# Kernel optimization log

Measured on AMD Instinct MI355X. Metric: run time of the kernel, lower is better.

Reference implementation:

```python
import jax, jax.numpy as jnp
import numpy as np

EPS = 1e-5

def layernorm(x, g, b):
    mu = jnp.mean(x, axis=-1, keepdims=True)
    var = jnp.mean((x - mu) ** 2, axis=-1, keepdims=True)
    return (x - mu) * jax.lax.rsqrt(var + EPS) * g + b

def cswin_attn(q, k, v, lepe_w, lepe_b, H, W, H_sp, W_sp, num_heads):
    # q,k,v: (B, L, C) with C = branch dim
    B, L, C = q.shape
    d = C // num_heads
    nH, nW = H // H_sp, W // W_sp
    def to_win(t):
        t = t.transpose(0, 2, 1).reshape(B, C, nH, H_sp, nW, W_sp)
        t = t.transpose(0, 2, 4, 3, 5, 1).reshape(B * nH * nW, H_sp * W_sp, num_heads, d)
        return t.transpose(0, 2, 1, 3)  # (Bw, h, N, d)
    kw = to_win(k)
    vw = to_win(v)
    # q windows as images for LePE depthwise conv
    qi = q.transpose(0, 2, 1).reshape(B, C, nH, H_sp, nW, W_sp)
    qi = qi.transpose(0, 2, 4, 1, 3, 5).reshape(B * nH * nW, C, H_sp, W_sp)
    lepe = jax.lax.conv_general_dilated(qi, lepe_w, (1, 1), 'SAME',
                                        feature_group_count=C,
                                        dimension_numbers=('NCHW', 'OIHW', 'NCHW'))
    lepe = lepe + lepe_b[None, :, None, None]
    lepe = lepe.reshape(-1, num_heads, d, H_sp * W_sp).transpose(0, 1, 3, 2)
    qw = qi.reshape(-1, num_heads, d, H_sp * W_sp).transpose(0, 1, 3, 2) * (float(d) ** -0.5)
    attn = jax.nn.softmax(jnp.einsum('whnd,whmd->whnm', qw, kw), axis=-1)
    out = jnp.einsum('whnm,whmd->whnd', attn, vw) + lepe  # (Bw, h, N, d)
    out = out.transpose(0, 2, 1, 3).reshape(B, nH, nW, H_sp, W_sp, C)
    out = out.transpose(0, 1, 3, 2, 4, 5).reshape(B, H * W, C)
    return out

def setup_inputs() -> dict:
    key = jax.random.key(0)
    ks = jax.random.split(key, 20)
    B, C, H, W = 8, 128, 64, 64
    ch_z = 512
    hid = 4 * C
    Cb = C // 2  # branch dim
    s = lambda fin: (1.0 / np.sqrt(fin))
    inp = {
        'x': jax.random.normal(ks[0], (B, C, H, W), jnp.float32),
        'z': jax.random.normal(ks[1], (B, ch_z), jnp.float32),
        'ln1_g': jnp.ones((C,), jnp.float32), 'ln1_b': jnp.zeros((C,), jnp.float32),
        'ln2_g': jnp.ones((C,), jnp.float32), 'ln2_b': jnp.zeros((C,), jnp.float32),
        'Wz1': jax.random.normal(ks[2], (C, ch_z), jnp.float32) * s(ch_z),
        'Wz2': jax.random.normal(ks[3], (C, ch_z), jnp.float32) * s(ch_z),
        'Wqkv': jax.random.normal(ks[4], (3 * C, C), jnp.float32) * s(C),
        'Wproj': jax.random.normal(ks[5], (C, C), jnp.float32) * s(C),
        'bproj': jnp.zeros((C,), jnp.float32),
        'lepe_w0': jax.random.normal(ks[6], (Cb, 1, 3, 3), jnp.float32) * (1.0 / 3.0),
        'lepe_b0': jnp.zeros((Cb,), jnp.float32),
        'lepe_w1': jax.random.normal(ks[7], (Cb, 1, 3, 3), jnp.float32) * (1.0 / 3.0),
        'lepe_b1': jnp.zeros((Cb,), jnp.float32),
        'W1': jax.random.normal(ks[8], (hid, C), jnp.float32) * s(C),
        'b1': jnp.zeros((hid,), jnp.float32),
        'W2': jax.random.normal(ks[9], (C, hid), jnp.float32) * s(hid),
        'b2': jnp.zeros((C,), jnp.float32),
    }
    return inp

def reference(x, z, ln1_g, ln1_b, ln2_g, ln2_b, Wz1, Wz2, Wqkv, Wproj, bproj,
              lepe_w0, lepe_b0, lepe_w1, lepe_b1, W1, b1, W2, b2):
    B, C, H, W = x.shape
    nh = 4  # num_heads // 2 per branch
    ss = 8  # split_size
    Cb = C // 2
    xf = x.reshape(B, C, H * W).transpose(0, 2, 1)  # (B, L, C)
    # code-conditioned attention branch
    z1 = z @ Wz1.T  # (B, C)
    h1 = layernorm(xf, ln1_g, ln1_b) + z1[:, None, :]
    qkv = (h1 @ Wqkv.T).reshape(B, H * W, 3, C).transpose(2, 0, 1, 3)  # (3, B, L, C)
    q, k, v = qkv[0], qkv[1], qkv[2]
    x1 = cswin_attn(q[..., :Cb], k[..., :Cb], v[..., :Cb], lepe_w0, lepe_b0, H, W, H, ss, nh)
    x2 = cswin_attn(q[..., Cb:], k[..., Cb:], v[..., Cb:], lepe_w1, lepe_b1, H, W, ss, W, nh)
    att = jnp.concatenate([x1, x2], axis=2) @ Wproj.T + bproj
    xf = xf + att
    # code-conditioned MLP branch
    z2 = z @ Wz2.T
    h2 = layernorm(xf, ln2_g, ln2_b) + z2[:, None, :]
    mlp = jax.nn.gelu(h2 @ W1.T + b1, approximate=False) @ W2.T + b2
    xf = xf + mlp
    return xf.transpose(0, 2, 1).reshape(B, C, H, W)
```

## Files before the change

### kernel.cpp

```cpp
#include <hip/hip_runtime.h>
#include <cstddef>

__device__ __forceinline__ float b2f(unsigned short u) {
  return __uint_as_float(((unsigned int)u) << 16);
}
__device__ __forceinline__ unsigned short f2b(float f) {
  unsigned int u = __float_as_uint(f);
  u = u + 0x7FFFu + ((u >> 16) & 1u);
  return (unsigned short)(u >> 16);
}
__device__ __forceinline__ unsigned int cvtpk(float lo, float hi) {
  unsigned int r;
  asm("v_cvt_pk_bf16_f32 %0, %1, %2" : "=v"(r) : "v"(lo), "v"(hi));
  return r;
}
__device__ __forceinline__ float gelu_exact(float x) {
  return 0.5f * x * (1.0f + erff(x * 0.70710678118654752f));
}

#if defined(__has_builtin)
#if __has_builtin(__builtin_amdgcn_exp2f)
#define EXP2(x) __builtin_amdgcn_exp2f(x)
#else
#define EXP2(x) __expf((x) * 0.6931471805599453f)
#endif
#else
#define EXP2(x) __expf((x) * 0.6931471805599453f)
#endif

typedef __attribute__((ext_vector_type(8))) short bf16x8;
typedef __attribute__((ext_vector_type(4))) float f32x4;

__device__ __forceinline__ unsigned int dtype_flag(const unsigned short* gref) {
  return (gref[0] == 0x3F80u) ? 1u : 0u;
}

struct Ptrs18 { const void* p[18]; };
__constant__ const int c_off[19] = {
    0, 4096, 4224, 4352, 4480, 4608, 70144, 135680, 184832, 201216,
    201344, 201920, 201984, 202560, 202624, 268160, 268672, 334208, 334336};

__global__ __launch_bounds__(256) void k_convert(Ptrs18 ptrs,
                                                 unsigned short* __restrict__ dst) {
  int idx = blockIdx.x * 256 + threadIdx.x;
  if (idx >= 334336) return;
  unsigned int flag = dtype_flag((const unsigned short*)ptrs.p[1]);
  int i = 0;
#pragma unroll
  for (int t = 1; t < 18; ++t) i += (idx >= c_off[t]);
  int local = idx - c_off[i];
  if (flag) dst[idx] = ((const unsigned short*)ptrs.p[i])[local];
  else      dst[idx] = f2b(((const float*)ptrs.p[i])[local]);
}

__global__ __launch_bounds__(256) void k_transpose_in(const void* __restrict__ x,
                                                      const unsigned short* __restrict__ gref,
                                                      float* __restrict__ xf) {
  __shared__ float t[32][33];
  unsigned int flag = dtype_flag(gref);
  int b = blockIdx.z;
  int l0 = blockIdx.x * 32, c0 = blockIdx.y * 32;
  int tx = threadIdx.x & 31, ty = threadIdx.x >> 5;
#pragma unroll
  for (int i = 0; i < 32; i += 8) {
    size_t gi = ((size_t)b * 128 + c0 + ty + i) * 4096 + l0 + tx;
    t[ty + i][tx] = flag ? b2f(((const unsigned short*)x)[gi]) : ((const float*)x)[gi];
  }
  __syncthreads();
#pragma unroll
  for (int i = 0; i < 32; i += 8)
    xf[((size_t)b * 4096 + l0 + ty + i) * 128 + c0 + tx] = t[tx][ty + i];
}

__global__ __launch_bounds__(256) void k_zmm(const unsigned short* __restrict__ z,
                                             const unsigned short* __restrict__ Wz1,
                                             const unsigned short* __restrict__ Wz2,
                                             float* __restrict__ zz) {
  __shared__ float sz[512];
  int b = blockIdx.x, tid = threadIdx.x;
  sz[tid]       = b2f(z[b * 512 + tid]);
  sz[tid + 256] = b2f(z[b * 512 + 256 + tid]);
  __syncthreads();
  const unsigned short* W = (tid < 128) ? Wz1 : Wz2;
  int c = tid & 127;
  const unsigned short* wr = W + c * 512;
  float acc = 0.f;
  for (int k = 0; k < 512; k += 4) {
    ushort4 wv = *(const ushort4*)&wr[k];
    acc += b2f(wv.x) * sz[k] + b2f(wv.y) * sz[k + 1] + b2f(wv.z) * sz[k + 2] + b2f(wv.w) * sz[k + 3];
  }
  zz[b * 256 + tid] = acc;
}

__global__ __launch_bounds__(256) void k_ln(const float* __restrict__ x,
                                            const unsigned short* __restrict__ g,
                                            const unsigned short* __restrict__ bb,
                                            const float* __restrict__ zz, int zsel,
                                            unsigned short* __restrict__ out) {
  int row = blockIdx.x * 4 + (threadIdx.x >> 6);
  int lane = threadIdx.x & 63;
  int b = row >> 12;
  const float* xr = x + (size_t)row * 128;
  float2 v = *(const float2*)&xr[lane * 2];
  float s = v.x + v.y, s2 = v.x * v.x + v.y * v.y;
#pragma unroll
  for (int m = 32; m; m >>= 1) {
    s += __shfl_xor(s, m, 64);
    s2 += __shfl_xor(s2, m, 64);
  }
  float mu = s * 0.0078125f;
  float var = s2 * 0.0078125f - mu * mu;
  float rstd = rsqrtf(var + 1e-5f);
  int c = lane * 2;
  const float* zr = zz + b * 256 + zsel * 128;
  float ox = (v.x - mu) * rstd * b2f(g[c])     + b2f(bb[c])     + zr[c];
  float oy = (v.y - mu) * rstd * b2f(g[c + 1]) + b2f(bb[c + 1]) + zr[c + 1];
  ushort2 o2; o2.x = f2b(ox); o2.y = f2b(oy);
  *(ushort2*)&out[(size_t)row * 128 + c] = o2;
}

__global__ __launch_bounds__(256) void k_gemm_mfma(const unsigned short* __restrict__ A,
                                                   const unsigned short* __restrict__ W,
                                                   const unsigned short* __restrict__ bias,
                                                   const float* __restrict__ res,
                                                   void* __restrict__ out,
                                                   int M, int N, int K, int ldw, int flags) {
  __shared__ unsigned short As[128][136];
  int bm = blockIdx.x * 128, bn = blockIdx.y * 128;
  int tid = threadIdx.x;
  int lane = tid & 63, wv = tid >> 6;
  int wm = (wv >> 1) * 64, wn = (wv & 1) * 64;
  int qd = lane >> 4, l15 = lane & 15;
#pragma unroll
  for (int i = tid; i < 2048; i += 256) {
    int row = i >> 4, c8 = (i & 15) << 3;
    *(bf16x8*)&As[row][c8] = *(const bf16x8*)&A[(size_t)(bm + row) * 128 + c8];
  }
  __syncthreads();
  f32x4 acc[4][4] = {};
#pragma unroll
  for (int ks = 0; ks < 4; ++ks) {
    bf16x8 af[4], bfr[4];
#pragma unroll
    for (int t = 0; t < 4; ++t) {
      af[t]  = *(const bf16x8*)&As[wm + t * 16 + l15][ks * 32 + qd * 8];
      bfr[t] = *(const bf16x8*)&W[(size_t)(bn + wn + t * 16 + l15) * ldw + ks * 32 + qd * 8];
    }
#pragma unroll
    for (int mi = 0; mi < 4; ++mi)
#pragma unroll
      for (int nj = 0; nj < 4; ++nj)
        acc[mi][nj] = __builtin_amdgcn_mfma_f32_16x16x32_bf16(af[mi], bfr[nj],
                                                              acc[mi][nj], 0, 0, 0);
  }
  if (flags & 4) {
#pragma unroll
    for (int mi = 0; mi < 4; ++mi)
#pragma unroll
      for (int r = 0; r < 4; ++r) {
        int row = bm + wm + mi * 16 + qd * 4 + r;
        int bb2 = row >> 12, l = row & 4095;
        int hI = l >> 6, wI = l & 63;
        int s0 = wI >> 3, t0 = hI * 8 + (wI & 7);
        int s1 = hI >> 3, t1 = (hI & 7) * 64 + wI;
#pragma unroll
        for (int nj = 0; nj < 4; ++nj) {
          int colb = bn + wn + nj * 16;
          int kv = colb >> 7, br = (colb >> 6) & 1, hh2 = (colb >> 4) & 3;
          int ss = br ? s1 : s0, tt = br ? t1 : t0;
          size_t addr = ((((size_t)((kv * 8 + bb2) * 2 + br) * 4 + hh2) * 8 + ss) * 512 + tt) * 16 + l15;
          ((unsigned short*)out)[addr] = f2b(acc[mi][nj][r]);
        }
      }
    return;
  }
  float bv[4];
#pragma unroll
  for (int nj = 0; nj < 4; ++nj)
    bv[nj] = bias ? b2f(bias[bn + wn + nj * 16 + l15]) : 0.f;
#pragma unroll
  for (int mi = 0; mi < 4; ++mi) {
#pragma unroll
    for (int r = 0; r < 4; ++r) {
      int row = bm + wm + mi * 16 + qd * 4 + r;
#pragma unroll
      for (int nj = 0; nj < 4; ++nj) {
        int col = bn + wn + nj * 16 + l15;
        float t = acc[mi][nj][r] + bv[nj];
        if (res) t += res[(size_t)row * N + col];
        if (flags & 2) ((unsigned short*)out)[(size_t)row * N + col] = f2b(t);
        else           ((float*)out)[(size_t)row * N + col] = t;
      }
    }
  }
}

__global__ __launch_bounds__(256, 4) void k_pm(const unsigned short* __restrict__ att,
                                               const unsigned short* __restrict__ Wp,
                                               const unsigned short* __restrict__ bp,
                                               const float* __restrict__ xf,
                                               const unsigned short* __restrict__ g,
                                               const unsigned short* __restrict__ bb,
                                               const float* __restrict__ zz,
                                               const unsigned short* __restrict__ W1,
                                               const unsigned short* __restrict__ b1,
                                               const unsigned short* __restrict__ W2,
                                               const unsigned short* __restrict__ b2,
                                               const unsigned short* __restrict__ gref,
                                               void* __restrict__ outp) {
  __shared__ __align__(16) char smem[35840];
  float (*xt)[132] = (float(*)[132])smem;
  unsigned short (*As_all)[136] = (unsigned short(*)[136])(smem + 16896);
  unsigned short (*Hs)[32][40]  = (unsigned short(*)[32][40])(smem + 25600);
  int tid = threadIdx.x;
  int bm = blockIdx.x * 32;
  int bidx = bm >> 12;
  int lane = tid & 63, wv = tid >> 6;
  int qd = lane >> 4, l15 = lane & 15;
  {
    int i = tid;
    int row = i >> 4, c8 = (i & 15) << 3;
    *(bf16x8*)&As_all[row][c8] = *(const bf16x8*)&att[(size_t)(bm + row) * 128 + c8];
    i += 256; row = i >> 4; c8 = (i & 15) << 3;
    *(bf16x8*)&As_all[row][c8] = *(const bf16x8*)&att[(size_t)(bm + row) * 128 + c8];
  }
  __syncthreads();
  {
    f32x4 acc[2][2] = {};
#pragma unroll
    for (int ks = 0; ks < 4; ++ks) {
      bf16x8 af[2], bfr[2];
#pragma unroll
      for (int t = 0; t < 2; ++t)
        af[t] = *(const bf16x8*)&As_all[t * 16 + l15][ks * 32 + qd * 8];
#pragma unroll
      for (int t = 0; t < 2; ++t)
        bfr[t] = *(const bf16x8*)&Wp[(wv * 32 + t * 16 + l15) * 128 + ks * 32 + qd * 8];
#pragma unroll
      for (int mi = 0; mi < 2; ++mi)
#pragma unroll
        for (int nj = 0; nj < 2; ++nj)
          acc[mi][nj] = __builtin_amdgcn_mfma_f32_16x16x32_bf16(af[mi], bfr[nj],
                                                                acc[mi][nj], 0, 0, 0);
    }
    float bv[2];
#pragma unroll
    for (int nj = 0; nj < 2; ++nj)
      bv[nj] = b2f(bp[wv * 32 + nj * 16 + l15]);
#pragma unroll
    for (int mi = 0; mi < 2; ++mi)
#pragma unroll
      for (int r = 0; r < 4; ++r) {
        int row = mi * 16 + qd * 4 + r;
#pragma unroll
        for (int nj = 0; nj < 2; ++nj) {
          int col = wv * 32 + nj * 16 + l15;
          xt[row][col] = acc[mi][nj][r] + bv[nj] + xf[(size_t)(bm + row) * 128 + col];
        }
      }
  }
  __syncthreads();
  {
    int row = tid >> 3, part = tid & 7;
    float v[16];
#pragma unroll
    for (int i = 0; i < 4; ++i) *(float4*)&v[i * 4] = *(const float4*)&xt[row][part * 16 + i * 4];
    float s = 0.f, s2 = 0.f;
#pragma unroll
    for (int i = 0; i < 16; ++i) { s += v[i]; s2 += v[i] * v[i]; }
    s  += __shfl_xor(s, 1, 64);  s  += __shfl_xor(s, 2, 64);  s  += __shfl_xor(s, 4, 64);
    s2 += __shfl_xor(s2, 1, 64); s2 += __shfl_xor(s2, 2, 64); s2 += __shfl_xor(s2, 4, 64);
    float mu = s * 0.0078125f;
    float var = s2 * 0.0078125f - mu * mu;
    float rstd = rsqrtf(var + 1e-5f);
    const float* zr = zz + bidx * 256 + 128 + part * 16;
#pragma unroll
    for (int i = 0; i < 16; i += 2) {
      int c = part * 16 + i;
      float ox = (v[i]     - mu) * rstd * b2f(g[c])     + b2f(bb[c])     + zr[i];
      float oy = (v[i + 1] - mu) * rstd * b2f(g[c + 1]) + b2f(bb[c + 1]) + zr[i + 1];
      unsigned int u = (unsigned int)f2b(ox) | ((unsigned int)f2b(oy) << 16);
      *(unsigned int*)&As_all[row][c] = u;
    }
  }
  __syncthreads();
  f32x4 acc2[2][2] = {};
#pragma unroll 1
  for (int j = 0; j < 4; ++j) {
    f32x4 acc1[2][2] = {};
    const unsigned short* W1j = W1 + j * 128 * 128;
#pragma unroll
    for (int ks = 0; ks < 4; ++ks) {
      bf16x8 af[2], bfr[2];
#pragma unroll
      for (int t = 0; t < 2; ++t)
        af[t] = *(const bf16x8*)&As_all[t * 16 + l15][ks * 32 + qd * 8];
#pragma unroll
      for (int t = 0; t < 2; ++t)
        bfr[t] = *(const bf16x8*)&W1j[(wv * 32 + t * 16 + l15) * 128 + ks * 32 + qd * 8];
#pragma unroll
      for (int mi = 0; mi < 2; ++mi)
#pragma unroll
        for (int nj = 0; nj < 2; ++nj)
          acc1[mi][nj] = __builtin_amdgcn_mfma_f32_16x16x32_bf16(af[mi], bfr[nj],
                                                                 acc1[mi][nj], 0, 0, 0);
    }
    if (j) __syncthreads();
    float bv1[2];
#pragma unroll
    for (int nj = 0; nj < 2; ++nj)
      bv1[nj] = b2f(b1[j * 128 + wv * 32 + nj * 16 + l15]);
#pragma unroll
    for (int mi = 0; mi < 2; ++mi)
#pragma unroll
      for (int nj = 0; nj < 2; ++nj)
#pragma unroll
        for (int r = 0; r < 4; ++r) {
          float t = gelu_exact(acc1[mi][nj][r] + bv1[nj]);
          Hs[wv][mi * 16 + qd * 4 + r][nj * 16 + l15] = f2b(t);
        }
    __syncthreads();
#pragma unroll
    for (int ks = 0; ks < 4; ++ks) {
      bf16x8 af2[2], bfr2[2];
#pragma unroll
      for (int t = 0; t < 2; ++t)
        af2[t] = *(const bf16x8*)&Hs[ks][t * 16 + l15][qd * 8];
#pragma unroll
      for (int t = 0; t < 2; ++t)
        bfr2[t] = *(const bf16x8*)&W2[(wv * 32 + t * 16 + l15) * 512 + j * 128 + ks * 32 + qd * 8];
#pragma unroll
      for (int mi = 0; mi < 2; ++mi)
#pragma unroll
        for (int nj = 0; nj < 2; ++nj)
          acc2[mi][nj] = __builtin_amdgcn_mfma_f32_16x16x32_bf16(af2[mi], bfr2[nj],
                                                                 acc2[mi][nj], 0, 0, 0);
    }
  }
  float bv2[2];
#pragma unroll
  for (int nj = 0; nj < 2; ++nj)
    bv2[nj] = b2f(b2[wv * 32 + nj * 16 + l15]);
  __syncthreads();
  float* tile = (float*)(smem + 16896);
#pragma unroll
  for (int mi = 0; mi < 2; ++mi)
#pragma unroll
    for (int r = 0; r < 4; ++r) {
      int row = mi * 16 + qd * 4 + r;
#pragma unroll
      for (int nj = 0; nj < 2; ++nj) {
        int col = wv * 32 + nj * 16 + l15;
        tile[col * 36 + row] = acc2[mi][nj][r] + bv2[nj] + xt[row][col];
      }
    }
  __syncthreads();
  unsigned int flag = dtype_flag(gref);
  int c = tid >> 1, hf = tid & 1;
  int b = bm >> 12, l0 = (bm & 4095) + hf * 16;
  const float* tr = &tile[c * 36 + hf * 16];
  if (flag) {
    unsigned short* op = (unsigned short*)outp + ((size_t)(b * 128 + c)) * 4096 + l0;
#pragma unroll
    for (int i = 0; i < 16; i += 4) {
      ushort4 o;
      o.x = f2b(tr[i]); o.y = f2b(tr[i + 1]); o.z = f2b(tr[i + 2]); o.w = f2b(tr[i + 3]);
      *(ushort4*)&op[i] = o;
    }
  } else {
    float* op = (float*)outp + ((size_t)(b * 128 + c)) * 4096 + l0;
#pragma unroll
    for (int i = 0; i < 16; i += 4)
      *(float4*)&op[i] = *(const float4*)&tr[i];
  }
}

__global__ __launch_bounds__(256, 4) void k_attn_mfma(const unsigned short* __restrict__ qkvw,
                                                      const unsigned short* __restrict__ lw0,
                                                      const unsigned short* __restrict__ lb0,
                                                      const unsigned short* __restrict__ lw1,
                                                      const unsigned short* __restrict__ lb1,
                                                      unsigned short* __restrict__ att) {
  __shared__ unsigned short Ks[512][16];
  __shared__ unsigned short Vt[16][520];
  const size_t S1 = 4194304;
  int branch = blockIdx.y;
  int bx = blockIdx.x;
  int half = bx & 1, wh = bx >> 1;
  int w = wh >> 2, hh = wh & 3;
  int b = w >> 3, s = w & 7;
  int cb = branch * 64 + hh * 16;
  size_t slab = ((size_t)(((b * 2 + branch) * 4 + hh) * 8 + s)) * 8192;
  const unsigned short* Qg = qkvw + slab;
  const unsigned short* Kg = qkvw + S1 + slab;
  const unsigned short* Vg = qkvw + 2 * S1 + slab;
  int tid = threadIdx.x;
  for (int i = tid; i < 1024; i += 256) {
    int tok = i >> 1, c8 = (i & 1) << 3;
    *(bf16x8*)&Ks[tok][c8] = *(const bf16x8*)&Kg[tok * 16 + c8];
    bf16x8 vv = *(const bf16x8*)&Vg[tok * 16 + c8];
    int col = (tok & ~31) | ((tok & 12) << 1) | ((tok & 16) >> 2) | (tok & 3);
#pragma unroll
    for (int j = 0; j < 8; ++j) Vt[c8 + j][col] = (unsigned short)vv[j];
  }
  __syncthreads();
  int lane = tid & 63, wv = tid >> 6;
  int qd = lane >> 4, l15 = lane & 15;
  int koff = (qd & 1) * 8;
  const unsigned short* lwp = branch ? lw1 : lw0;
  const unsigned short* lbp = branch ? lb1 : lb0;
  float wreg[4][9], breg[4];
#pragma unroll
  for (int r = 0; r < 4; ++r) {
    int cc = hh * 16 + qd * 4 + r;
    breg[r] = b2f(lbp[cc]);
#pragma unroll
    for (int j = 0; j < 9; ++j) wreg[r][j] = b2f(lwp[cc * 9 + j]);
  }
  bf16x8 onesv;
#pragma unroll
  for (int j = 0; j < 8; ++j) onesv[j] = (short)0x3F80;
  int sy = branch ? 64 : 8;
  int yl = branch ? 8 : 64;
  int xl = branch ? 64 : 8;
  const float QSCALE = 0.25f * 1.44269504f;
  const float NS = -11.5415603f;
  const f32x4 NSHIFT = {NS, NS, NS, NS};
#pragma unroll 1
  for (int qt = 0; qt < 4; ++qt) {
    int q0 = half * 256 + wv * 64 + qt * 16;
    int tq = q0 + l15;
    bf16x8 qf = {};
    if (qd < 2) {
      bf16x8 raw = *(const bf16x8*)&Qg[tq * 16 + qd * 8];
#pragma unroll
      for (int j = 0; j < 8; ++j)
        qf[j] = (short)f2b(b2f((unsigned short)raw[j]) * QSCALE);
    }
    f32x4 O0 = {0.f, 0.f, 0.f, 0.f}, O1 = {0.f, 0.f, 0.f, 0.f};
    f32x4 Osum = {0.f, 0.f, 0.f, 0.f};
#pragma unroll 1
    for (int kc = 0; kc < 4; ++kc) {
      f32x4 sc[8];
#pragma unroll
      for (int c = 0; c < 8; ++c) {
        bf16x8 kf = *(const bf16x8*)&Ks[kc * 128 + c * 16 + l15][koff];
        sc[c] = __builtin_amdgcn_mfma_f32_16x16x32_bf16(kf, qf, NSHIFT, 0, 0, 0);
      }
#pragma unroll
      for (int c = 0; c < 8; ++c) {
        float e0 = EXP2(sc[c][0]), e1 = EXP2(sc[c][1]);
        float e2 = EXP2(sc[c][2]), e3 = EXP2(sc[c][3]);
        sc[c][0] = __uint_as_float(cvtpk(e0, e1));
        sc[c][1] = __uint_as_float(cvtpk(e2, e3));
      }
#pragma unroll
      for (int bc = 0; bc < 4; ++bc) {
        union { unsigned int u[4]; bf16x8 v; } pu;
        pu.u[0] = __float_as_uint(sc[2 * bc][0]);
        pu.u[1] = __float_as_uint(sc[2 * bc][1]);
        pu.u[2] = __float_as_uint(sc[2 * bc + 1][0]);
        pu.u[3] = __float_as_uint(sc[2 * bc + 1][1]);
        bf16x8 vf = *(const bf16x8*)&Vt[l15][kc * 128 + bc * 32 + qd * 8];
        Osum = __builtin_amdgcn_mfma_f32_16x16x32_bf16(onesv, pu.v, Osum, 0, 0, 0);
        if (bc & 1) O1 = __builtin_amdgcn_mfma_f32_16x16x32_bf16(vf, pu.v, O1, 0, 0, 0);
        else        O0 = __builtin_amdgcn_mfma_f32_16x16x32_bf16(vf, pu.v, O0, 0, 0, 0);
      }
    }
    int y = branch ? (tq >> 6) : (tq >> 3);
    int x = branch ? (tq & 63) : (tq & 7);
    float lep[4] = {breg[0], breg[1], breg[2], breg[3]};
#pragma unroll
    for (int dy = -1; dy <= 1; ++dy)
#pragma unroll
      for (int dx = -1; dx <= 1; ++dx) {
        if ((unsigned)(y + dy) < (unsigned)yl && (unsigned)(x + dx) < (unsigned)xl) {
          int tn = tq + dy * sy + dx;
          int j = (dy + 1) * 3 + (dx + 1);
          ushort4 qv = *(const ushort4*)&Qg[tn * 16 + qd * 4];
          lep[0] += wreg[0][j] * b2f(qv.x);
          lep[1] += wreg[1][j] * b2f(qv.y);
          lep[2] += wreg[2][j] * b2f(qv.z);
          lep[3] += wreg[3][j] * b2f(qv.w);
        }
      }
    float inv = 1.f / Osum[0];
    int lo = branch ? (s * 8 + y) * 64 + x : y * 64 + s * 8 + x;
    unsigned short* op = att + ((size_t)(b * 4096 + lo)) * 128 + cb + qd * 4;
    ushort4 o;
    o.x = f2b((O0[0] + O1[0]) * inv + lep[0]);
    o.y = f2b((O0[1] + O1[1]) * inv + lep[1]);
    o.z = f2b((O0[2] + O1[2]) * inv + lep[2]);
    o.w = f2b((O0[3] + O1[3]) * inv + lep[3]);
    *(ushort4*)op = o;
  }
}

extern "C" void kernel_launch(void* const* d_in, const int* in_sizes, int n_in,
                              void* d_out, int out_size, void* d_ws, size_t ws_size,
                              hipStream_t stream) {
  const size_t S = 4194304;
  float* ws = (float*)d_ws;
  float* zz = ws + 64;
  unsigned short* norm = (unsigned short*)(ws + 2112);
  float* xf = ws + 169472;
  unsigned short* h   = (unsigned short*)(ws + 169472 + S);
  unsigned short* qkv = (unsigned short*)(ws + 169472 + S + S / 2);
  unsigned short* att = h;

  const unsigned short* z     = norm + 0;
  const unsigned short* ln1g  = norm + 4096;
  const unsigned short* ln1b  = norm + 4224;
  const unsigned short* ln2g  = norm + 4352;
  const unsigned short* ln2b  = norm + 4480;
  const unsigned short* Wz1   = norm + 4608;
  const unsigned short* Wz2   = norm + 70144;
  const unsigned short* Wqkv  = norm + 135680;
  const unsigned short* Wproj = norm + 184832;
  const unsigned short* bproj = norm + 201216;
  const unsigned short* lw0   = norm + 201344;
  const unsigned short* lb0   = norm + 201920;
  const unsigned short* lw1   = norm + 201984;
  const unsigned short* lb1   = norm + 202560;
  const unsigned short* W1    = norm + 202624;
  const unsigned short* b1    = norm + 268160;
  const unsigned short* W2    = norm + 268672;
  const unsigned short* b2    = norm + 334208;

  const unsigned short* gref = (const unsigned short*)d_in[2];

  Ptrs18 ptrs;
  for (int i = 0; i < 18; ++i) ptrs.p[i] = d_in[i + 1];

  dim3 t256(256);
  k_convert<<<dim3(1306), t256, 0, stream>>>(ptrs, (unsigned short*)norm);
  k_transpose_in<<<dim3(128, 4, 8), t256, 0, stream>>>(d_in[0], gref, xf);
  k_zmm<<<dim3(8), t256, 0, stream>>>(z, Wz1, Wz2, zz);
  k_ln<<<dim3(8192), t256, 0, stream>>>(xf, ln1g, ln1b, zz, 0, h);
  k_gemm_mfma<<<dim3(256, 3), t256, 0, stream>>>(h, Wqkv, nullptr, nullptr, qkv,
                                                 32768, 384, 128, 128, 2 | 4);
  k_attn_mfma<<<dim3(512, 2), t256, 0, stream>>>(qkv, lw0, lb0, lw1, lb1, att);
  k_pm<<<dim3(1024), t256, 0, stream>>>(att, Wproj, bproj, xf, ln2g, ln2b, zz,
                                        W1, b1, W2, b2, gref, d_out);
}
```

Measured before the change: 216.1 us.

## Merge convert and transpose kernels, hoist W2 loads, use K=16 MFMA for QK

Merges the weight-conversion and input-transpose kernels into a single launch, with the grid split by block index, which removes one kernel launch. In the MLP kernel, the W2 fragment loads are issued before the barrier and GELU stage so their latency is hidden, at the cost of more registers. In attention, the QK score MFMA with head dim 16 now uses a 16x16x16 bf16 instruction instead of a zero-padded 16x16x32 one, which avoids the wasted half of the instruction.

```diff
diff --git a/kernel.cpp b/kernel.cpp
--- a/kernel.cpp
+++ b/kernel.cpp
@@ -29,7 +29,18 @@
 #endif
 
 typedef __attribute__((ext_vector_type(8))) short bf16x8;
+typedef __attribute__((ext_vector_type(4))) short bf16x4;
 typedef __attribute__((ext_vector_type(4))) float f32x4;
+
+#if defined(__has_builtin)
+#if __has_builtin(__builtin_amdgcn_mfma_f32_16x16x16bf16_1k)
+#define MFMA16(a, b, c) __builtin_amdgcn_mfma_f32_16x16x16bf16_1k(a, b, c, 0, 0, 0)
+#define HAVE_MFMA16 1
+#elif __has_builtin(__builtin_amdgcn_mfma_f32_16x16x16_bf16)
+#define MFMA16(a, b, c) __builtin_amdgcn_mfma_f32_16x16x16_bf16(a, b, c, 0, 0, 0)
+#define HAVE_MFMA16 1
+#endif
+#endif
 
 __device__ __forceinline__ unsigned int dtype_flag(const unsigned short* gref) {
   return (gref[0] == 0x3F80u) ? 1u : 0u;
@@ -40,26 +51,29 @@
     0, 4096, 4224, 4352, 4480, 4608, 70144, 135680, 184832, 201216,
     201344, 201920, 201984, 202560, 202624, 268160, 268672, 334208, 334336};
 
-__global__ __launch_bounds__(256) void k_convert(Ptrs18 ptrs,
-                                                 unsigned short* __restrict__ dst) {
-  int idx = blockIdx.x * 256 + threadIdx.x;
-  if (idx >= 334336) return;
-  unsigned int flag = dtype_flag((const unsigned short*)ptrs.p[1]);
-  int i = 0;
-#pragma unroll
-  for (int t = 1; t < 18; ++t) i += (idx >= c_off[t]);
-  int local = idx - c_off[i];
-  if (flag) dst[idx] = ((const unsigned short*)ptrs.p[i])[local];
-  else      dst[idx] = f2b(((const float*)ptrs.p[i])[local]);
-}
-
-__global__ __launch_bounds__(256) void k_transpose_in(const void* __restrict__ x,
-                                                      const unsigned short* __restrict__ gref,
-                                                      float* __restrict__ xf) {
+__global__ __launch_bounds__(256) void k_front(Ptrs18 ptrs,
+                                               unsigned short* __restrict__ dst,
+                                               const void* __restrict__ x,
+                                               const unsigned short* __restrict__ gref,
+                                               float* __restrict__ xf) {
   __shared__ float t[32][33];
+  int bx = blockIdx.x;
+  if (bx < 1306) {
+    int idx = bx * 256 + threadIdx.x;
+    if (idx >= 334336) return;
+    unsigned int flag = dtype_flag((const unsigned short*)ptrs.p[1]);
+    int i = 0;
+#pragma unroll
+    for (int tt = 1; tt < 18; ++tt) i += (idx >= c_off[tt]);
+    int local = idx - c_off[i];
+    if (flag) dst[idx] = ((const unsigned short*)ptrs.p[i])[local];
+    else      dst[idx] = f2b(((const float*)ptrs.p[i])[local]);
+    return;
+  }
+  int lb = bx - 1306;
   unsigned int flag = dtype_flag(gref);
-  int b = blockIdx.z;
-  int l0 = blockIdx.x * 32, c0 = blockIdx.y * 32;
+  int b = lb >> 9;
+  int c0 = ((lb >> 7) & 3) * 32, l0 = (lb & 127) * 32;
   int tx = threadIdx.x & 31, ty = threadIdx.x >> 5;
 #pragma unroll
   for (int i = 0; i < 32; i += 8) {
@@ -305,6 +319,12 @@
           acc1[mi][nj] = __builtin_amdgcn_mfma_f32_16x16x32_bf16(af[mi], bfr[nj],
                                                                  acc1[mi][nj], 0, 0, 0);
     }
+    bf16x8 w2f[8];
+#pragma unroll
+    for (int ks = 0; ks < 4; ++ks)
+#pragma unroll
+      for (int t = 0; t < 2; ++t)
+        w2f[ks * 2 + t] = *(const bf16x8*)&W2[(wv * 32 + t * 16 + l15) * 512 + j * 128 + ks * 32 + qd * 8];
     if (j) __syncthreads();
     float bv1[2];
 #pragma unroll
@@ -322,18 +342,15 @@
     __syncthreads();
 #pragma unroll
     for (int ks = 0; ks < 4; ++ks) {
-      bf16x8 af2[2], bfr2[2];
+      bf16x8 af2[2];
 #pragma unroll
       for (int t = 0; t < 2; ++t)
         af2[t] = *(const bf16x8*)&Hs[ks][t * 16 + l15][qd * 8];
 #pragma unroll
-      for (int t = 0; t < 2; ++t)
-        bfr2[t] = *(const bf16x8*)&W2[(wv * 32 + t * 16 + l15) * 512 + j * 128 + ks * 32 + qd * 8];
-#pragma unroll
       for (int mi = 0; mi < 2; ++mi)
 #pragma unroll
         for (int nj = 0; nj < 2; ++nj)
-          acc2[mi][nj] = __builtin_amdgcn_mfma_f32_16x16x32_bf16(af2[mi], bfr2[nj],
+          acc2[mi][nj] = __builtin_amdgcn_mfma_f32_16x16x32_bf16(af2[mi], w2f[ks * 2 + nj],
                                                                  acc2[mi][nj], 0, 0, 0);
     }
   }
@@ -430,6 +447,16 @@
   for (int qt = 0; qt < 4; ++qt) {
     int q0 = half * 256 + wv * 64 + qt * 16;
     int tq = q0 + l15;
+#ifdef HAVE_MFMA16
+    bf16x4 qf;
+    {
+      ushort4 raw = *(const ushort4*)&Qg[tq * 16 + qd * 4];
+      qf[0] = (short)f2b(b2f(raw.x) * QSCALE);
+      qf[1] = (short)f2b(b2f(raw.y) * QSCALE);
+      qf[2] = (short)f2b(b2f(raw.z) * QSCALE);
+      qf[3] = (short)f2b(b2f(raw.w) * QSCALE);
+    }
+#else
     bf16x8 qf = {};
     if (qd < 2) {
       bf16x8 raw = *(const bf16x8*)&Qg[tq * 16 + qd * 8];
@@ -437,6 +464,7 @@
       for (int j = 0; j < 8; ++j)
         qf[j] = (short)f2b(b2f((unsigned short)raw[j]) * QSCALE);
     }
+#endif
     f32x4 O0 = {0.f, 0.f, 0.f, 0.f}, O1 = {0.f, 0.f, 0.f, 0.f};
     f32x4 Osum = {0.f, 0.f, 0.f, 0.f};
 #pragma unroll 1
@@ -444,8 +472,13 @@
       f32x4 sc[8];
 #pragma unroll
       for (int c = 0; c < 8; ++c) {
+#ifdef HAVE_MFMA16
+        bf16x4 kf = *(const bf16x4*)&Ks[kc * 128 + c * 16 + l15][qd * 4];
+        sc[c] = MFMA16(kf, qf, NSHIFT);
+#else
         bf16x8 kf = *(const bf16x8*)&Ks[kc * 128 + c * 16 + l15][koff];
         sc[c] = __builtin_amdgcn_mfma_f32_16x16x32_bf16(kf, qf, NSHIFT, 0, 0, 0);
+#endif
       }
 #pragma unroll
       for (int c = 0; c < 8; ++c) {
@@ -533,8 +566,8 @@
   for (int i = 0; i < 18; ++i) ptrs.p[i] = d_in[i + 1];
 
   dim3 t256(256);
-  k_convert<<<dim3(1306), t256, 0, stream>>>(ptrs, (unsigned short*)norm);
-  k_transpose_in<<<dim3(128, 4, 8), t256, 0, stream>>>(d_in[0], gref, xf);
+  k_front<<<dim3(5402), t256, 0, stream>>>(ptrs, (unsigned short*)norm,
+                                           d_in[0], gref, xf);
   k_zmm<<<dim3(8), t256, 0, stream>>>(z, Wz1, Wz2, zz);
   k_ln<<<dim3(8192), t256, 0, stream>>>(xf, ln1g, ln1b, zz, 0, h);
   k_gemm_mfma<<<dim3(256, 3), t256, 0, stream>>>(h, Wqkv, nullptr, nullptr, qkv,
```

Measured after the change: 215.1 us (median of 2 runs). About the same (-0.4%).
